# Kernel tuning notes

Hardware: AMD Instinct MI355X
Metric: run time of the kernel (lower is better)

## Reference

```python
import jax, jax.numpy as jnp
import numpy as np

N, D, C, K, M = 32768, 512, 64, 16, 128
DEPTH = 4            # log2(K): decision-tree depth per codebook
NODES = K - 1        # 15 internal tree nodes per codebook


def _build_selection_matrix():
    # Node i of the binary tree lives at level log2(i+1) and thresholds the
    # level-l selected dimension of its codebook.
    S = np.zeros((C * NODES, C * DEPTH), dtype=np.float32)
    base = np.zeros((NODES, DEPTH), dtype=np.float32)
    for i in range(NODES):
        base[i, int(np.log2(i + 1))] = 1.0
    for c in range(C):
        S[c * NODES:(c + 1) * NODES, c * DEPTH:(c + 1) * DEPTH] = base
    return S


def _build_bit_matrix():
    # Leaf k scores +1/-1 on each of its DEPTH ancestor nodes; the true leaf
    # attains the maximal score DEPTH.
    base = np.zeros((K, NODES), dtype=np.float32)
    for k in range(K):
        for l in range(DEPTH):
            node = (1 << l) - 1 + (k >> (DEPTH - l))   # ancestor at level l
            bit = (k >> (DEPTH - 1 - l)) & 1            # right(1)/left(0)
            base[k, node] = 1.0 if bit else -1.0
    B = np.zeros((C * K, C * NODES), dtype=np.float32)
    for c in range(C):
        B[c * K:(c + 1) * K, c * NODES:(c + 1) * NODES] = base
    return B


def setup_inputs() -> dict:
    key = jax.random.key(0)
    k1, k2, k3, k4 = jax.random.split(key, 4)
    I = jax.random.normal(k1, (N, D), jnp.float32)
    T = jax.random.normal(k2, (C * NODES,), jnp.float32) * 0.1   # thresholds
    L = jax.random.normal(k3, (M, C, K), jnp.float32)            # LUT
    dims = jnp.sort(jax.random.randint(k4, (C * DEPTH,), 0, D))  # selected cols
    S = jnp.asarray(_build_selection_matrix())
    B = jnp.asarray(_build_bit_matrix())
    temp = jnp.ones((1,), jnp.float32)
    return {"I": I, "T": T, "L": L, "S": S, "B": B, "dims": dims, "temp": temp}


def reference(I, T, L, S, B, dims, temp):
    t = temp[0]
    x_sel = I[:, dims]                                  # (N, C*DEPTH) gather
    h = x_sel @ S.T - T                                 # (N, C*NODES)
    tanh_h = jnp.tanh(h / t)
    # straight-through sign: forward sign(h), backward d(tanh(h/t))
    sign_ste = jnp.sign(h) - jax.lax.stop_gradient(tanh_h) + tanh_h
    b = sign_ste @ B.T                                  # (N, C*K) leaf scores
    soft = jax.nn.softmax(b.reshape(-1, C, K) / t, axis=2)
    hard = jax.nn.one_hot(jnp.argmax(soft, axis=2), K, dtype=soft.dtype)
    # straight-through one-hot encoding E: forward hard, backward soft
    E = hard - jax.lax.stop_gradient(soft) + soft       # (N, C, K)
    return jnp.einsum("nck,mck->nm", E, L)              # LUT gather-sum readout
```

## Files before the change

kernel.cpp:

```cpp
#include <hip/hip_runtime.h>

#define N_TOTAL 32768
#define D_DIM   512
#define C_DIM   64
#define K_DIM   16
#define M_DIM   128
#define NODES_  15
#define ROWS    16

typedef unsigned short u16;
typedef unsigned int   u32;
typedef unsigned long long u64;
typedef unsigned char  u8;
typedef float  f32x4  __attribute__((ext_vector_type(4)));
typedef short  short8v __attribute__((ext_vector_type(8)));

__device__ __forceinline__ u32 f2bf_bits(float f) {
    u32 u = __float_as_uint(f);
    return (u + 0x7FFFu + ((u >> 16) & 1u)) >> 16;
}

__device__ __forceinline__ void gload_lds16(const float* g, float* l) {
    __builtin_amdgcn_global_load_lds(
        (const __attribute__((address_space(1))) void*)g,
        (__attribute__((address_space(3))) void*)l, 16, 0, 0);
}

__global__ __launch_bounds__(256) void build_lbf(
    const float* __restrict__ L, u16* __restrict__ Lbf)
{
    int idx  = blockIdx.x * 256 + threadIdx.x;
    int lane = idx & 63;
    int ch   = (idx >> 6) & 31;
    int ct   = idx >> 11;
    int m  = ct * 16 + (lane & 15);
    int k0 = ch * 32 + ((lane >> 4) * 8);
    const float* src = L + (size_t)m * 1024 + k0;
    float4 a = *(const float4*)(src);
    float4 b = *(const float4*)(src + 4);
    u32 w0 = f2bf_bits(a.x) | (f2bf_bits(a.y) << 16);
    u32 w1 = f2bf_bits(a.z) | (f2bf_bits(a.w) << 16);
    u32 w2 = f2bf_bits(b.x) | (f2bf_bits(b.y) << 16);
    u32 w3 = f2bf_bits(b.z) | (f2bf_bits(b.w) << 16);
    *(uint4*)(Lbf + (size_t)idx * 8) = make_uint4(w0, w1, w2, w3);
}

__global__ __launch_bounds__(256) void codes_kernel(
    const float* __restrict__ I,
    const float* __restrict__ T,
    const int* __restrict__ dims,
    u8* __restrict__ cws)
{
    __shared__ float sI[ROWS * D_DIM];
    __shared__ float sT[C_DIM * NODES_];

    const int tid  = threadIdx.x;
    const int lane = tid & 63;
    const int wv   = tid >> 6;
    const int rowBase = blockIdx.x * ROWS + wv * 4;

    {
        const float* src = I + (size_t)rowBase * D_DIM;
        float* dst = sI + wv * 4 * D_DIM;
        #pragma unroll
        for (int i = 0; i < 8; ++i)
            gload_lds16(src + i * 256 + lane * 4, dst + i * 256);
    }

    const int4 dml = ((const int4*)dims)[lane];

    for (int j = tid; j < C_DIM * NODES_; j += 256) sT[j] = T[j];
    __syncthreads();

    const float* tc = sT + lane * NODES_;
    u32 cp = 0;
    #pragma unroll
    for (int rr = 0; rr < 4; ++rr) {
        const float* v = sI + (wv * 4 + rr) * D_DIM;
        float x0 = v[dml.x], x1 = v[dml.y], x2 = v[dml.z], x3 = v[dml.w];
        int node = 0, k = 0;
        int b0 = (x0 - tc[0] > 0.0f) ? 1 : 0;
        k = b0; node = 1 + b0;
        int b1 = (x1 - tc[node] > 0.0f) ? 1 : 0;
        k = (k << 1) | b1; node = (node << 1) + 1 + b1;
        int b2 = (x2 - tc[node] > 0.0f) ? 1 : 0;
        k = (k << 1) | b2; node = (node << 1) + 1 + b2;
        int b3 = (x3 - tc[node] > 0.0f) ? 1 : 0;
        k = (k << 1) | b3;
        cp |= (u32)k << (4 * rr);
    }

    u32 cw =  (cp & 0xFu)
           | ((cp >> 4)  & 0xFu) << 8
           | ((cp >> 8)  & 0xFu) << 16
           | ((cp >> 12) & 0xFu) << 24;
    *(u32*)(cws + (size_t)lane * N_TOTAL + rowBase) = cw;
}

__global__ __launch_bounds__(256) void gemm_kernel(
    const u16* __restrict__ Lbf,
    const u8* __restrict__ cws,
    float* __restrict__ out)
{
    __shared__ u8 sC[C_DIM * 64];

    const int tid  = threadIdx.x;
    const int lane = tid & 63;
    const int wv   = tid >> 6;
    const int rowBase = blockIdx.x * 64;

    {
        int cls = tid >> 2, off = (tid & 3) * 16;
        *(uint4*)(sC + cls * 64 + off) =
            *(const uint4*)(cws + (size_t)cls * N_TOTAL + rowBase + off);
    }
    __syncthreads();

    const int l15     = lane & 15;
    const int clsLane = (lane >> 5) & 1;
    const int kb      = ((lane >> 4) & 1) * 8;

    f32x4 acc[4][2] = {};

    const u16* lb0 = Lbf + ((size_t)(wv * 2 + 0) * 32 * 64 + lane) * 8;
    const u16* lb1 = Lbf + ((size_t)(wv * 2 + 1) * 32 * 64 + lane) * 8;

    #pragma unroll 4
    for (int ch = 0; ch < 32; ++ch) {
        union { uint4 u; short8v v; } b0, b1;
        b0.u = *(const uint4*)(lb0 + (size_t)ch * 64 * 8);
        b1.u = *(const uint4*)(lb1 + (size_t)ch * 64 * 8);
        const int cls = ch * 2 + clsLane;
        #pragma unroll
        for (int rt = 0; rt < 4; ++rt) {
            u32 cd = sC[cls * 64 + rt * 16 + l15];
            u32 tt = cd - (u32)kb;
            u64 sv = 0x3F80ull << ((tt & 3) * 16);
            union { u64 d[2]; short8v v; } a;
            a.d[0] = (tt < 4) ? sv : 0ull;
            a.d[1] = (tt >= 4 && tt < 8) ? sv : 0ull;
            acc[rt][0] = __builtin_amdgcn_mfma_f32_16x16x32_bf16(
                             a.v, b0.v, acc[rt][0], 0, 0, 0);
            acc[rt][1] = __builtin_amdgcn_mfma_f32_16x16x32_bf16(
                             a.v, b1.v, acc[rt][1], 0, 0, 0);
        }
    }

    #pragma unroll
    for (int rt = 0; rt < 4; ++rt) {
        #pragma unroll
        for (int cj = 0; cj < 2; ++cj) {
            int col = (wv * 2 + cj) * 16 + l15;
            int r0  = rowBase + rt * 16 + ((lane >> 4) << 2);
            float* o = out + (size_t)r0 * M_DIM + col;
            o[0 * M_DIM] = acc[rt][cj][0];
            o[1 * M_DIM] = acc[rt][cj][1];
            o[2 * M_DIM] = acc[rt][cj][2];
            o[3 * M_DIM] = acc[rt][cj][3];
        }
    }
}

extern "C" void kernel_launch(void* const* d_in, const int* in_sizes, int n_in,
                              void* d_out, int out_size, void* d_ws, size_t ws_size,
                              hipStream_t stream) {
    const float* I    = (const float*)d_in[0];
    const float* T    = (const float*)d_in[1];
    const float* L    = (const float*)d_in[2];
    const int*   dims = (const int*)d_in[5];

    u16* Lbf = (u16*)d_ws;
    u8*  cw  = (u8*)d_ws + (1 << 18);

    hipLaunchKernelGGL(build_lbf, dim3(64), dim3(256), 0, stream, L, Lbf);
    hipLaunchKernelGGL(codes_kernel, dim3(N_TOTAL / ROWS), dim3(256), 0, stream,
                       I, T, dims, cw);
    hipLaunchKernelGGL(gemm_kernel, dim3(N_TOTAL / 64), dim3(256), 0, stream,
                       Lbf, cw, (float*)d_out);
}
```

Measured before the change: 129.8 us.

## Fuse tree-code computation into the LUT GEMM kernel and drop the codes buffer

Merges the separate codes kernel into the MFMA GEMM kernel. Each block now computes the tree codes for its own 64 rows in four 16-row chunks, reusing one shared-memory tile for the input rows, and writes the codes packed per lane into shared memory instead of a global buffer. This removes one kernel launch and the global write and read of the code buffer. The GEMM reads four codes with a single 32-bit shared-memory load instead of four byte loads. In exchange, each block streams its input rows serially with a vmcnt wait between chunks, and the grid is smaller, so memory latency may be less hidden.

After: 120.2 us. 1.08x faster.

```diff
diff --git a/kernel.cpp b/kernel.cpp
--- a/kernel.cpp
+++ b/kernel.cpp
@@ -6,13 +6,12 @@
 #define K_DIM   16
 #define M_DIM   128
 #define NODES_  15
-#define ROWS    16
 
 typedef unsigned short u16;
 typedef unsigned int   u32;
 typedef unsigned long long u64;
 typedef unsigned char  u8;
-typedef float  f32x4  __attribute__((ext_vector_type(4)));
+typedef float  f32x4   __attribute__((ext_vector_type(4)));
 typedef short  short8v __attribute__((ext_vector_type(8)));
 
 __device__ __forceinline__ u32 f2bf_bits(float f) {
@@ -45,74 +44,65 @@
     *(uint4*)(Lbf + (size_t)idx * 8) = make_uint4(w0, w1, w2, w3);
 }
 
-__global__ __launch_bounds__(256) void codes_kernel(
+__global__ __launch_bounds__(256) void mega_kernel(
     const float* __restrict__ I,
     const float* __restrict__ T,
     const int* __restrict__ dims,
-    u8* __restrict__ cws)
-{
-    __shared__ float sI[ROWS * D_DIM];
-    __shared__ float sT[C_DIM * NODES_];
-
-    const int tid  = threadIdx.x;
-    const int lane = tid & 63;
-    const int wv   = tid >> 6;
-    const int rowBase = blockIdx.x * ROWS + wv * 4;
-
-    {
-        const float* src = I + (size_t)rowBase * D_DIM;
-        float* dst = sI + wv * 4 * D_DIM;
-        #pragma unroll
-        for (int i = 0; i < 8; ++i)
-            gload_lds16(src + i * 256 + lane * 4, dst + i * 256);
-    }
-
-    const int4 dml = ((const int4*)dims)[lane];
-
-    for (int j = tid; j < C_DIM * NODES_; j += 256) sT[j] = T[j];
-    __syncthreads();
-
-    const float* tc = sT + lane * NODES_;
-    u32 cp = 0;
-    #pragma unroll
-    for (int rr = 0; rr < 4; ++rr) {
-        const float* v = sI + (wv * 4 + rr) * D_DIM;
-        float x0 = v[dml.x], x1 = v[dml.y], x2 = v[dml.z], x3 = v[dml.w];
-        int node = 0, k = 0;
-        int b0 = (x0 - tc[0] > 0.0f) ? 1 : 0;
-        k = b0; node = 1 + b0;
-        int b1 = (x1 - tc[node] > 0.0f) ? 1 : 0;
-        k = (k << 1) | b1; node = (node << 1) + 1 + b1;
-        int b2 = (x2 - tc[node] > 0.0f) ? 1 : 0;
-        k = (k << 1) | b2; node = (node << 1) + 1 + b2;
-        int b3 = (x3 - tc[node] > 0.0f) ? 1 : 0;
-        k = (k << 1) | b3;
-        cp |= (u32)k << (4 * rr);
-    }
-
-    u32 cw =  (cp & 0xFu)
-           | ((cp >> 4)  & 0xFu) << 8
-           | ((cp >> 8)  & 0xFu) << 16
-           | ((cp >> 12) & 0xFu) << 24;
-    *(u32*)(cws + (size_t)lane * N_TOTAL + rowBase) = cw;
-}
-
-__global__ __launch_bounds__(256) void gemm_kernel(
     const u16* __restrict__ Lbf,
-    const u8* __restrict__ cws,
     float* __restrict__ out)
 {
-    __shared__ u8 sC[C_DIM * 64];
+    __shared__ float sI[16 * D_DIM];
+    __shared__ float sT[C_DIM * NODES_];
+    __shared__ u8    sC2[C_DIM * 16 * 4];
 
     const int tid  = threadIdx.x;
     const int lane = tid & 63;
     const int wv   = tid >> 6;
     const int rowBase = blockIdx.x * 64;
 
+    const int4 dml = ((const int4*)dims)[lane];
+
     {
-        int cls = tid >> 2, off = (tid & 3) * 16;
-        *(uint4*)(sC + cls * 64 + off) =
-            *(const uint4*)(cws + (size_t)cls * N_TOTAL + rowBase + off);
+        const float* src = I + (size_t)(rowBase + wv * 4) * D_DIM;
+        float* dst = sI + wv * 4 * D_DIM;
+        #pragma unroll
+        for (int i = 0; i < 8; ++i)
+            gload_lds16(src + i * 256 + lane * 4, dst + i * 256);
+    }
+    for (int j = tid; j < C_DIM * NODES_; j += 256) sT[j] = T[j];
+    __syncthreads();
+
+    const float* tc = sT + lane * NODES_;
+
+    #pragma unroll
+    for (int ci = 0; ci < 4; ++ci) {
+        if (ci) asm volatile("s_waitcnt vmcnt(0)" ::: "memory");
+        u32 cp = 0;
+        #pragma unroll
+        for (int rr = 0; rr < 4; ++rr) {
+            const float* v = sI + (wv * 4 + rr) * D_DIM;
+            float x0 = v[dml.x], x1 = v[dml.y], x2 = v[dml.z], x3 = v[dml.w];
+            int node = 0, k = 0;
+            int b0 = (x0 - tc[0] > 0.0f) ? 1 : 0;
+            k = b0; node = 1 + b0;
+            int b1 = (x1 - tc[node] > 0.0f) ? 1 : 0;
+            k = (k << 1) | b1; node = (node << 1) + 1 + b1;
+            int b2 = (x2 - tc[node] > 0.0f) ? 1 : 0;
+            k = (k << 1) | b2; node = (node << 1) + 1 + b2;
+            int b3 = (x3 - tc[node] > 0.0f) ? 1 : 0;
+            k = (k << 1) | b3;
+            cp |= (u32)k << (4 * rr);
+        }
+        #pragma unroll
+        for (int rr = 0; rr < 4; ++rr)
+            sC2[lane * 64 + (wv * 4 + rr) * 4 + ci] = (cp >> (4 * rr)) & 15u;
+        if (ci < 3) {
+            const float* src = I + (size_t)(rowBase + (ci + 1) * 16 + wv * 4) * D_DIM;
+            float* dst = sI + wv * 4 * D_DIM;
+            #pragma unroll
+            for (int i = 0; i < 8; ++i)
+                gload_lds16(src + i * 256 + lane * 4, dst + i * 256);
+        }
     }
     __syncthreads();
 
@@ -131,9 +121,10 @@
         b0.u = *(const uint4*)(lb0 + (size_t)ch * 64 * 8);
         b1.u = *(const uint4*)(lb1 + (size_t)ch * 64 * 8);
         const int cls = ch * 2 + clsLane;
+        const u32 codes4 = *(const u32*)(sC2 + cls * 64 + l15 * 4);
         #pragma unroll
         for (int rt = 0; rt < 4; ++rt) {
-            u32 cd = sC[cls * 64 + rt * 16 + l15];
+            u32 cd = (codes4 >> (8 * rt)) & 0xFFu;
             u32 tt = cd - (u32)kb;
             u64 sv = 0x3F80ull << ((tt & 3) * 16);
             union { u64 d[2]; short8v v; } a;
@@ -170,11 +161,8 @@
     const int*   dims = (const int*)d_in[5];
 
     u16* Lbf = (u16*)d_ws;
-    u8*  cw  = (u8*)d_ws + (1 << 18);
 
     hipLaunchKernelGGL(build_lbf, dim3(64), dim3(256), 0, stream, L, Lbf);
-    hipLaunchKernelGGL(codes_kernel, dim3(N_TOTAL / ROWS), dim3(256), 0, stream,
-                       I, T, dims, cw);
-    hipLaunchKernelGGL(gemm_kernel, dim3(N_TOTAL / 64), dim3(256), 0, stream,
-                       Lbf, cw, (float*)d_out);
+    hipLaunchKernelGGL(mega_kernel, dim3(N_TOTAL / 64), dim3(256), 0, stream,
+                       I, T, dims, Lbf, (float*)d_out);
 }
```
